# Kernel tuning notes

Measured on AMD Instinct MI355X. Metric: run time of the kernel, lower is better.

Reference implementation:

```python
import jax, jax.numpy as jnp
import numpy as np

INPUT_DIM = 362
HIDDEN = 256
STYLE_NUM = 60
OUTFIT_NUM = 49710
BATCH = 16384


def setup_inputs() -> dict:
    key = jax.random.key(0)
    ks = jax.random.split(key, 12)
    f32 = jnp.float32
    return {
        "i_feature": jax.random.normal(ks[0], (BATCH, INPUT_DIM), f32),
        "j_feature": jax.random.normal(ks[1], (BATCH, INPUT_DIM), f32),
        "k_feature": jax.random.normal(ks[2], (BATCH, INPUT_DIM), f32),
        # top_emb / bottom_emb Linear params (stored transposed: x @ W + b)
        "W_top": jax.random.normal(ks[3], (INPUT_DIM, HIDDEN), f32) * 0.05,
        "b_top": jnp.zeros((HIDDEN,), f32),
        "W_bot": jax.random.normal(ks[4], (INPUT_DIM, HIDDEN), f32) * 0.05,
        "b_bot": jnp.zeros((HIDDEN,), f32),
        # NMF factors (forward relu_'s them in place; we relu on use)
        "P_nmf": jax.random.normal(ks[5], (2 * INPUT_DIM, STYLE_NUM), f32),
        "N_nmf": jax.random.normal(ks[6], (2 * INPUT_DIM, STYLE_NUM), f32),
        "H1_nmf": jax.random.normal(ks[7], (STYLE_NUM, OUTFIT_NUM), f32),
        "H2_nmf": jax.random.normal(ks[8], (STYLE_NUM, OUTFIT_NUM), f32),
        "matirx_pos": jax.random.uniform(ks[9], (2 * INPUT_DIM, OUTFIT_NUM), f32),
        "matirx_neg": jax.random.uniform(ks[10], (2 * INPUT_DIM, OUTFIT_NUM), f32),
    }


def _emb(x, W, b):
    # nn.Sequential(Linear, Sigmoid)
    return jax.nn.sigmoid(x @ W + b)


def _style_score(i_f, j_f, styles, W_top, b_top, W_bot, b_bot):
    # Vectorized version of the per-sample loop:
    # squared-distance argmin codebook lookup + gather + rowwise dot.
    outfit = jnp.concatenate([i_f, j_f], axis=1)  # [B, 2D]
    # mean over feature dim of (x - s)^2; constant 1/(2D) scale does not change argmin
    d2 = (jnp.sum(outfit * outfit, axis=1, keepdims=True)
          - 2.0 * (outfit @ styles)
          + jnp.sum(styles * styles, axis=0, keepdims=True))  # [B, S]
    idx = jnp.argmin(d2, axis=1)                               # [B]
    sel = styles.T[idx]                                        # [B, 2D] gather
    top, bot = sel[:, :INPUT_DIM], sel[:, INPUT_DIM:]
    # diag(matmul) == rowwise dot
    return jnp.sum(_emb(top, W_top, b_top) * _emb(bot, W_bot, b_bot), axis=1)  # [B]


def reference(i_feature, j_feature, k_feature, W_top, b_top, W_bot, b_bot,
              P_nmf, N_nmf, H1_nmf, H2_nmf, matirx_pos, matirx_neg):
    Ti = _emb(i_feature, W_top, b_top)   # [B, H]
    Bj = _emb(j_feature, W_bot, b_bot)   # [B, H]
    Bk = _emb(k_feature, W_bot, b_bot)   # [B, H]
    # torch.diag(matmul(Ti, Bj.T)) == rowwise dot (avoids [B,B] intermediate)
    ij_score = jnp.sum(Ti * Bj, axis=1)  # [B]
    ik_score = jnp.sum(Ti * Bk, axis=1)  # [B]

    # forward does relu_ on .data before use
    P = jnp.maximum(P_nmf, 0.0)
    N = jnp.maximum(N_nmf, 0.0)
    H1 = jnp.maximum(H1_nmf, 0.0)
    H2 = jnp.maximum(H2_nmf, 0.0)

    style_ij = _style_score(i_feature, j_feature, P, W_top, b_top, W_bot, b_bot)
    style_ik = _style_score(i_feature, k_feature, N, W_top, b_top, W_bot, b_bot)

    # -mean(log(sigmoid(d))) computed stably
    loss1 = -jnp.mean(jax.nn.log_sigmoid(ij_score - ik_score))
    loss2 = -jnp.mean(jax.nn.log_sigmoid(style_ij - style_ik))
    loss3 = jnp.mean(jnp.square(matirx_pos - P @ H1)
                     + jnp.square(matirx_neg - N @ H2))
    loss = loss1 + loss2 + 0.1 * loss3

    ij_ik = jnp.stack([ij_score, ik_score], axis=1)  # [B, 2]
    auc = jnp.mean((jnp.argmax(ij_ik, axis=1) == 0).astype(jnp.float32))
    return (loss, loss1, loss2, loss3, auc)
```

## Files before the change

kernel.cpp:

```cpp
#include <hip/hip_runtime.h>
#include <math.h>

#define BATCH 16384
#define IND   362
#define KP    384
#define HID   256
#define STY   60
#define NOUT  49710
#define OUTP  49920
#define D2    724
#define D2P   768

#define NB_SS   120
#define NB_HR   3120
#define NB_CW   768
#define NB_CPN  384
#define NB_CF   9216
#define NB_PREP (NB_SS + NB_HR + NB_CW + NB_CPN + NB_CF)

#define NB_HH   16
#define NB_PPB  2
#define NB_HEAD (NB_HH + NB_PPB)
#define N_DT    46
#define N_OC    24
#define OCHUNK  2080
#define NB_M    (2 * N_DT * N_OC)
#define NB_EMB  1024
#define NB_SA   512
#define NB_MAIN (NB_HEAD + NB_M + NB_EMB + NB_SA)

typedef __bf16 bf16x8 __attribute__((ext_vector_type(8)));
typedef float  floatx4 __attribute__((ext_vector_type(4)));
typedef float  floatx2 __attribute__((ext_vector_type(2)));

__device__ inline floatx4 mfma16(bf16x8 a, bf16x8 b, floatx4 c) {
  return __builtin_amdgcn_mfma_f32_16x16x32_bf16(a, b, c, 0, 0, 0);
}

__device__ inline unsigned short f32_to_bf16(float x) {
  unsigned int u = __float_as_uint(x);
  unsigned int r = (u + 0x7FFFu + ((u >> 16) & 1u)) >> 16;
  return (unsigned short)r;
}

__device__ inline float sigm_fast(float x) { return 1.0f / (1.0f + __expf(-x)); }
__device__ inline float softplusf(float z) { return fmaxf(z, 0.0f) + log1pf(expf(-fabsf(z))); }

__global__ __launch_bounds__(256) void k_prep(
    const float* __restrict__ fi, const float* __restrict__ fj, const float* __restrict__ fk,
    const float* __restrict__ Wt, const float* __restrict__ btop,
    const float* __restrict__ Wb, const float* __restrict__ bbot,
    const float* __restrict__ Pn, const float* __restrict__ Nn,
    const float* __restrict__ H1, const float* __restrict__ H2,
    unsigned short* __restrict__ fbf, unsigned short* __restrict__ wbfT,
    unsigned short* __restrict__ pnbfT, unsigned short* __restrict__ hrows,
    float* __restrict__ ss, float* __restrict__ cn) {
  __shared__ float sel[D2];
  __shared__ float shr[4];
  int b = blockIdx.x;
  int t = threadIdx.x;

  if (b < NB_SS) {
    int s  = b % STY;
    int mt = b / STY;
    const float* M = mt ? Nn : Pn;
    float cnp = 0.0f;
    for (int d = t; d < D2; d += 256) {
      float v = fmaxf(M[(size_t)d * STY + s], 0.0f);
      sel[d] = v;
      cnp += v * v;
    }
    __syncthreads();
    float at = btop[t], ab = bbot[t];
    for (int d = 0; d < IND; d++) at = fmaf(sel[d],       Wt[(size_t)d * HID + t], at);
    for (int d = 0; d < IND; d++) ab = fmaf(sel[IND + d], Wb[(size_t)d * HID + t], ab);
    float prod = (1.0f / (1.0f + expf(-at))) * (1.0f / (1.0f + expf(-ab)));
    for (int off = 32; off > 0; off >>= 1) prod += __shfl_xor(prod, off);
    if ((t & 63) == 0) shr[t >> 6] = prod;
    __syncthreads();
    if (t == 0) ss[mt * 64 + s] = shr[0] + shr[1] + shr[2] + shr[3];
    __syncthreads();
    for (int off = 32; off > 0; off >>= 1) cnp += __shfl_xor(cnp, off);
    if ((t & 63) == 0) shr[t >> 6] = cnp;
    __syncthreads();
    if (t == 0) cn[mt * 64 + s] = shr[0] + shr[1] + shr[2] + shr[3];
    return;
  }
  b -= NB_SS;

  if (b < NB_HR) {
    int e = (b * 256 + t) * 8;
    int row = e / OUTP;
    int o = e - row * OUTP;
    int s = row & 63;
    int mm = row >> 6;
    const float* H = mm ? H2 : H1;
    unsigned short* dst = hrows + (size_t)row * OUTP + o;
    unsigned int wv[4];
    if (s < STY && o + 8 <= NOUT) {
      const float* src = H + (size_t)s * NOUT + o;
      #pragma unroll
      for (int ee = 0; ee < 4; ee++) {
        floatx2 v = *(const floatx2*)(src + 2 * ee);
        wv[ee] = (unsigned)f32_to_bf16(fmaxf(v[0], 0.0f)) |
                 ((unsigned)f32_to_bf16(fmaxf(v[1], 0.0f)) << 16);
      }
    } else {
      #pragma unroll
      for (int ee = 0; ee < 4; ee++) {
        float lo = (s < STY && o + 2 * ee     < NOUT) ? fmaxf(H[(size_t)s * NOUT + o + 2 * ee],     0.0f) : 0.0f;
        float hi = (s < STY && o + 2 * ee + 1 < NOUT) ? fmaxf(H[(size_t)s * NOUT + o + 2 * ee + 1], 0.0f) : 0.0f;
        wv[ee] = (unsigned)f32_to_bf16(lo) | ((unsigned)f32_to_bf16(hi) << 16);
      }
    }
    uint4 v; v.x = wv[0]; v.y = wv[1]; v.z = wv[2]; v.w = wv[3];
    *(uint4*)dst = v;
    return;
  }
  b -= NB_HR;

  if (b < NB_CW) {
    int idx = b * 256 + t;
    int k = idx % KP;
    int rem = idx / KP;
    int h = rem % HID;
    int mm = rem / HID;
    const float* W = mm ? Wb : Wt;
    wbfT[idx] = f32_to_bf16(k < IND ? W[(size_t)k * HID + h] : 0.0f);
    return;
  }
  b -= NB_CW;

  if (b < NB_CPN) {
    int u = b * 256 + t;
    int s = u & 63;
    int v = u >> 6;
    int m = (v >= D2P) ? 1 : 0;
    int d = v - m * D2P;
    const float* M = m ? Nn : Pn;
    float x = (d < D2 && s < STY) ? fmaxf(M[(size_t)d * STY + s], 0.0f) : 0.0f;
    unsigned short bb = f32_to_bf16(x);
    int k = (d < IND) ? d : (d < D2 ? d + 22 : (d < 746 ? d - IND : d));
    pnbfT[((size_t)m * 64 + s) * D2P + k] = bb;
    return;
  }
  b -= NB_CPN;

  {
    long u = (long)b * 256 + t;
    int g = (int)(u % 48);
    long rf = u / 48;
    int row = (int)(rf % BATCH);
    int f = (int)(rf / BATCH);
    const float* src = (f == 0) ? fi : (f == 1 ? fj : fk);
    int d0 = g * 8;
    const float* sp = src + (size_t)row * IND + d0;
    unsigned int wv[4];
    #pragma unroll
    for (int e = 0; e < 4; e++) {
      int dd = d0 + 2 * e;
      float lo = (dd < IND)     ? sp[2 * e]     : 0.0f;
      float hi = (dd + 1 < IND) ? sp[2 * e + 1] : 0.0f;
      wv[e] = (unsigned)f32_to_bf16(lo) | ((unsigned)f32_to_bf16(hi) << 16);
    }
    uint4 v; v.x = wv[0]; v.y = wv[1]; v.z = wv[2]; v.w = wv[3];
    *(uint4*)(fbf + ((size_t)f * BATCH + row) * KP + d0) = v;
  }
}

__global__ __launch_bounds__(256, 4) void k_main(
    const unsigned short* __restrict__ fbf, const unsigned short* __restrict__ wbfT,
    const unsigned short* __restrict__ pnbfT, const unsigned short* __restrict__ hrows,
    const float* __restrict__ btop, const float* __restrict__ bbot,
    const float* __restrict__ cn, const float* __restrict__ ss,
    const float* __restrict__ mp, const float* __restrict__ mneg,
    const float* __restrict__ Pn, const float* __restrict__ Nn,
    float* __restrict__ sIJ, float* __restrict__ sIK,
    float* __restrict__ stIJ, float* __restrict__ stIK,
    float* __restrict__ HHb, float* __restrict__ PPb,
    float* __restrict__ partial) {
  __shared__ float shp[4];
  __shared__ float red[4096];
  int w = threadIdx.x >> 6, lane = threadIdx.x & 63;
  int m = lane & 15, q = lane >> 4;
  int b = blockIdx.x;

  if (b < NB_HEAD) {
    bool isPP = (b >= NB_HH);
    int mat, chunk, nsteps, stride;
    const unsigned short* Rb;
    if (!isPP) { mat = b >> 3; chunk = b & 7; Rb = hrows + (size_t)mat * 64 * OUTP; stride = OUTP; nsteps = 195; }
    else       { mat = b - NB_HH; chunk = 0; Rb = pnbfT + (size_t)mat * 64 * D2P;  stride = D2P;  nsteps = 24;  }
    const unsigned short* Rm = Rb + (size_t)m * stride;

    floatx4 acc[4][4];
    #pragma unroll
    for (int a2 = 0; a2 < 4; a2++)
      #pragma unroll
      for (int b2 = 0; b2 < 4; b2++) acc[a2][b2] = (floatx4){0.f, 0.f, 0.f, 0.f};

    bf16x8 hc[4], hn[4];
    auto LD = [&](int j, bf16x8* h) {
      int k = (chunk * nsteps + j) * 32 + q * 8;
      #pragma unroll
      for (int st = 0; st < 4; st++)
        h[st] = *(const bf16x8*)(Rm + (size_t)(st * 16) * stride + k);
    };
    int j = w;
    LD(j, hc);
    for (; j < nsteps; j += 4) {
      if (j + 4 < nsteps) LD(j + 4, hn);
      #pragma unroll
      for (int a2 = 0; a2 < 4; a2++)
        #pragma unroll
        for (int b2 = 0; b2 < 4; b2++)
          acc[a2][b2] = mfma16(hc[a2], hc[b2], acc[a2][b2]);
      #pragma unroll
      for (int st = 0; st < 4; st++) hc[st] = hn[st];
    }
    for (int idx = threadIdx.x; idx < 4096; idx += 256) red[idx] = 0.f;
    __syncthreads();
    #pragma unroll
    for (int a2 = 0; a2 < 4; a2++)
      #pragma unroll
      for (int b2 = 0; b2 < 4; b2++)
        #pragma unroll
        for (int r = 0; r < 4; r++)
          atomicAdd(&red[(a2 * 16 + q * 4 + r) * 64 + b2 * 16 + m], acc[a2][b2][r]);
    __syncthreads();
    float* dst = (isPP ? PPb : HHb) + (size_t)mat * 4096;
    for (int idx = threadIdx.x; idx < 4096; idx += 256) atomicAdd(&dst[idx], red[idx]);
    return;
  }
  b -= NB_HEAD;

  if (b < NB_M) {
    int dt  = b % N_DT;
    int r   = b / N_DT;
    int oc  = r % N_OC;
    int mat = r / N_OC;
    int d0 = dt * 16, o0 = oc * OCHUNK;
    bool full = (o0 + OCHUNK <= NOUT);
    int d = d0 + m;
    bool rowok = (d < D2);
    const float* Mrow = (mat ? mneg : mp) + (size_t)d * NOUT;
    const unsigned short* Hbase = hrows + ((size_t)mat * 64 + m) * OUTP;

    floatx4 acc[4];
    #pragma unroll
    for (int st = 0; st < 4; st++) acc[st] = (floatx4){0.f, 0.f, 0.f, 0.f};
    float msq = 0.0f;

    floatx2 mc[4], mnx[4];
    bf16x8  hc[4], hn[4];

    auto LOADM = [&](int j, floatx2* dst) {
      int o = o0 + j * 32 + q * 8;
      if (rowok) {
        const float* Mr = Mrow + o;
        if (full) {
          dst[0] = *(const floatx2*)(Mr);
          dst[1] = *(const floatx2*)(Mr + 2);
          dst[2] = *(const floatx2*)(Mr + 4);
          dst[3] = *(const floatx2*)(Mr + 6);
        } else {
          #pragma unroll
          for (int e = 0; e < 4; e++) {
            floatx2 v = {0.f, 0.f};
            if (o + 2 * e     < NOUT) v[0] = Mr[2 * e];
            if (o + 2 * e + 1 < NOUT) v[1] = Mr[2 * e + 1];
            dst[e] = v;
          }
        }
      } else {
        #pragma unroll
        for (int e = 0; e < 4; e++) dst[e] = (floatx2){0.f, 0.f};
      }
    };
    auto LOADH = [&](int j, bf16x8* h) {
      int o = o0 + j * 32 + q * 8;
      #pragma unroll
      for (int st = 0; st < 4; st++)
        h[st] = *(const bf16x8*)(Hbase + (size_t)(st * 16) * OUTP + o);
    };

    LOADM(w, mc);
    LOADH(w, hc);
    for (int j = w; j < 65; j += 4) {
      if (j + 4 < 65) { LOADM(j + 4, mnx); LOADH(j + 4, hn); }
      union { unsigned int u32[4]; bf16x8 v; } cv;
      #pragma unroll
      for (int e = 0; e < 4; e++) {
        msq = fmaf(mc[e][0], mc[e][0], msq);
        msq = fmaf(mc[e][1], mc[e][1], msq);
        cv.u32[e] = (unsigned)f32_to_bf16(mc[e][0]) | ((unsigned)f32_to_bf16(mc[e][1]) << 16);
      }
      bf16x8 af = cv.v;
      #pragma unroll
      for (int st = 0; st < 4; st++) acc[st] = mfma16(af, hc[st], acc[st]);
      #pragma unroll
      for (int e = 0; e < 4; e++) mc[e] = mnx[e];
      #pragma unroll
      for (int st = 0; st < 4; st++) hc[st] = hn[st];
    }

    const float* PM = mat ? Nn : Pn;
    float t2 = 0.0f;
    #pragma unroll
    for (int st = 0; st < 4; st++) {
      int s = st * 16 + m;
      if (s < STY) {
        #pragma unroll
        for (int rg = 0; rg < 4; rg++) {
          int dd = d0 + q * 4 + rg;
          if (dd < D2) {
            float pv = fmaxf(PM[(size_t)dd * STY + s], 0.0f);
            t2 = fmaf(pv, acc[st][rg], t2);
          }
        }
      }
    }
    float local = msq - 2.0f * t2;
    for (int off = 32; off > 0; off >>= 1) local += __shfl_xor(local, off);
    if (lane == 0) shp[w] = local;
    __syncthreads();
    if (threadIdx.x == 0) partial[b] = shp[0] + shp[1] + shp[2] + shp[3];
    return;
  }
  b -= NB_M;

  if (b < NB_EMB) {
    int r0 = (b & 255) * 64 + w * 16;
    int hb = (b >> 8) * 64;
    const unsigned short* fi = fbf + (size_t)(r0 + m) * KP + q * 8;
    const unsigned short* fj = fi + (size_t)BATCH * KP;
    const unsigned short* fk = fj + (size_t)BATCH * KP;
    floatx4 accI[4], accJ[4], accK[4];
    #pragma unroll
    for (int nt = 0; nt < 4; nt++) {
      accI[nt] = (floatx4){0.f, 0.f, 0.f, 0.f};
      accJ[nt] = (floatx4){0.f, 0.f, 0.f, 0.f};
      accK[nt] = (floatx4){0.f, 0.f, 0.f, 0.f};
    }
    for (int kc = 0; kc < 12; kc++) {
      bf16x8 ai = *(const bf16x8*)(fi + kc * 32);
      bf16x8 aj = *(const bf16x8*)(fj + kc * 32);
      bf16x8 ak = *(const bf16x8*)(fk + kc * 32);
      #pragma unroll
      for (int nt = 0; nt < 4; nt++) {
        int n = hb + nt * 16 + m;
        const unsigned short* wp = wbfT + (size_t)n * KP + kc * 32 + q * 8;
        bf16x8 bt8 = *(const bf16x8*)(wp);
        bf16x8 bb8 = *(const bf16x8*)(wp + (size_t)HID * KP);
        accI[nt] = mfma16(ai, bt8, accI[nt]);
        accJ[nt] = mfma16(aj, bb8, accJ[nt]);
        accK[nt] = mfma16(ak, bb8, accK[nt]);
      }
    }
    float sij[4] = {0.f, 0.f, 0.f, 0.f}, sik[4] = {0.f, 0.f, 0.f, 0.f};
    #pragma unroll
    for (int nt = 0; nt < 4; nt++) {
      int n = hb + nt * 16 + m;
      float vbt = btop[n], vbb = bbot[n];
      #pragma unroll
      for (int reg = 0; reg < 4; reg++) {
        float ti = sigm_fast(accI[nt][reg] + vbt);
        float tj = sigm_fast(accJ[nt][reg] + vbb);
        float tk = sigm_fast(accK[nt][reg] + vbb);
        sij[reg] += ti * tj;
        sik[reg] += ti * tk;
      }
    }
    #pragma unroll
    for (int reg = 0; reg < 4; reg++) {
      for (int off = 1; off < 16; off <<= 1) {
        sij[reg] += __shfl_xor(sij[reg], off);
        sik[reg] += __shfl_xor(sik[reg], off);
      }
    }
    if (m == 0) {
      #pragma unroll
      for (int reg = 0; reg < 4; reg++) {
        int row = r0 + q * 4 + reg;
        atomicAdd(&sIJ[row], sij[reg]);
        atomicAdd(&sIK[row], sik[reg]);
      }
    }
    return;
  }
  b -= NB_EMB;

  {
    int mat = w & 1;
    int r0 = b * 32 + (w >> 1) * 16;
    const unsigned short* fA = fbf + (size_t)(r0 + m) * KP + q * 8;
    const unsigned short* fB = fA + (size_t)(1 + mat) * BATCH * KP;
    const unsigned short* Bp = pnbfT + (size_t)mat * 64 * D2P + q * 8;
    floatx4 acc[4];
    #pragma unroll
    for (int nt = 0; nt < 4; nt++) acc[nt] = (floatx4){0.f, 0.f, 0.f, 0.f};
    for (int kc = 0; kc < 24; kc++) {
      bf16x8 a = (kc < 12) ? *(const bf16x8*)(fA + kc * 32)
                           : *(const bf16x8*)(fB + (kc - 12) * 32);
      #pragma unroll
      for (int nt = 0; nt < 4; nt++) {
        bf16x8 bb = *(const bf16x8*)(Bp + (size_t)(nt * 16 + m) * D2P + kc * 32);
        acc[nt] = mfma16(a, bb, acc[nt]);
      }
    }
    const float* cnm = cn + mat * 64;
    float bv[4]; int bi[4];
    #pragma unroll
    for (int reg = 0; reg < 4; reg++) { bv[reg] = __builtin_inff(); bi[reg] = 1 << 30; }
    #pragma unroll
    for (int nt = 0; nt < 4; nt++) {
      int s = nt * 16 + m;
      float c = cnm[s & 63];
      #pragma unroll
      for (int reg = 0; reg < 4; reg++) {
        float d2 = (s < STY) ? (c - 2.0f * acc[nt][reg]) : __builtin_inff();
        if (d2 < bv[reg] || (d2 == bv[reg] && s < bi[reg])) { bv[reg] = d2; bi[reg] = s; }
      }
    }
    for (int off = 1; off < 16; off <<= 1) {
      #pragma unroll
      for (int reg = 0; reg < 4; reg++) {
        float ov = __shfl_xor(bv[reg], off);
        int   oi = __shfl_xor(bi[reg], off);
        if (ov < bv[reg] || (ov == bv[reg] && oi < bi[reg])) { bv[reg] = ov; bi[reg] = oi; }
      }
    }
    if (m == 0) {
      float* dst = mat ? stIK : stIJ;
      const float* ssm = ss + mat * 64;
      #pragma unroll
      for (int reg = 0; reg < 4; reg++) dst[r0 + q * 4 + reg] = ssm[bi[reg]];
    }
  }
}

__global__ __launch_bounds__(256) void k_final(
    const float* __restrict__ sIJ, const float* __restrict__ sIK,
    const float* __restrict__ stIJ, const float* __restrict__ stIK,
    const float* __restrict__ l3partial,
    const float* __restrict__ HHb, const float* __restrict__ PPb,
    float* __restrict__ out) {
  int t = threadIdx.x;
  float l1 = 0.f, l2 = 0.f, ac = 0.f;
  for (int r = t; r < BATCH; r += 256) {
    float dij = sIJ[r] - sIK[r];
    l1 += softplusf(-dij);
    if (dij >= 0.0f) ac += 1.0f;
    float dst = stIJ[r] - stIK[r];
    l2 += softplusf(-dst);
  }
  double l3 = 0.0;
  for (int p = t; p < NB_M; p += 256) l3 += (double)l3partial[p];
  for (int idx = t; idx < 8192; idx += 256) l3 += (double)HHb[idx] * (double)PPb[idx];
  __shared__ float sh1[4], sh2[4], sh3[4];
  __shared__ double sh4[4];
  for (int off = 32; off > 0; off >>= 1) {
    l1 += __shfl_xor(l1, off);
    l2 += __shfl_xor(l2, off);
    ac += __shfl_xor(ac, off);
    l3 += __shfl_xor(l3, off);
  }
  if ((t & 63) == 0) { sh1[t >> 6] = l1; sh2[t >> 6] = l2; sh3[t >> 6] = ac; sh4[t >> 6] = l3; }
  __syncthreads();
  if (t == 0) {
    double L1 = 0, L2 = 0, AC = 0, L3 = 0;
    for (int i = 0; i < 4; i++) { L1 += sh1[i]; L2 += sh2[i]; AC += sh3[i]; L3 += sh4[i]; }
    L1 /= BATCH; L2 /= BATCH; AC /= BATCH;
    L3 /= ((double)D2 * (double)NOUT);
    out[0] = (float)(L1 + L2 + 0.1 * L3);
    out[1] = (float)L1;
    out[2] = (float)L2;
    out[3] = (float)L3;
    out[4] = (float)AC;
  }
}

extern "C" void kernel_launch(void* const* d_in, const int* in_sizes, int n_in,
                              void* d_out, int out_size, void* d_ws, size_t ws_size,
                              hipStream_t stream) {
  (void)in_sizes; (void)n_in; (void)out_size; (void)ws_size;
  const float* i_f  = (const float*)d_in[0];
  const float* j_f  = (const float*)d_in[1];
  const float* k_f  = (const float*)d_in[2];
  const float* W_t  = (const float*)d_in[3];
  const float* b_t  = (const float*)d_in[4];
  const float* W_b  = (const float*)d_in[5];
  const float* b_b  = (const float*)d_in[6];
  const float* P_n  = (const float*)d_in[7];
  const float* N_n  = (const float*)d_in[8];
  const float* H1   = (const float*)d_in[9];
  const float* H2   = (const float*)d_in[10];
  const float* Mp   = (const float*)d_in[11];
  const float* Mn   = (const float*)d_in[12];
  float* out = (float*)d_out;
  char* ws = (char*)d_ws;

  const size_t OFF_FBF   = 0;
  const size_t OFF_WBFT  = OFF_FBF   + (size_t)3 * BATCH * KP * 2;
  const size_t OFF_PNBFT = OFF_WBFT  + (size_t)2 * HID * KP * 2;
  const size_t OFF_HROWS = OFF_PNBFT + (size_t)2 * 64 * D2P * 2;
  const size_t OFF_SIJ   = OFF_HROWS + (size_t)2 * 64 * OUTP * 2;
  const size_t OFF_SIK   = OFF_SIJ   + (size_t)BATCH * 4;
  const size_t OFF_HH    = OFF_SIK   + (size_t)BATCH * 4;
  const size_t OFF_PP    = OFF_HH    + (size_t)2 * 4096 * 4;
  const size_t OFF_STIJ  = OFF_PP    + (size_t)2 * 4096 * 4;
  const size_t OFF_STIK  = OFF_STIJ  + (size_t)BATCH * 4;
  const size_t OFF_SS    = OFF_STIK  + (size_t)BATCH * 4;
  const size_t OFF_CN    = OFF_SS    + 512;
  const size_t OFF_L3P   = OFF_CN    + 512;

  unsigned short* fbf   = (unsigned short*)(ws + OFF_FBF);
  unsigned short* wbfT  = (unsigned short*)(ws + OFF_WBFT);
  unsigned short* pnbfT = (unsigned short*)(ws + OFF_PNBFT);
  unsigned short* hrows = (unsigned short*)(ws + OFF_HROWS);
  float*  sIJ  = (float*)(ws + OFF_SIJ);
  float*  sIK  = (float*)(ws + OFF_SIK);
  float*  HHb  = (float*)(ws + OFF_HH);
  float*  PPb  = (float*)(ws + OFF_PP);
  float*  stIJ = (float*)(ws + OFF_STIJ);
  float*  stIK = (float*)(ws + OFF_STIK);
  float*  ss   = (float*)(ws + OFF_SS);
  float*  cn   = (float*)(ws + OFF_CN);
  float*  l3p  = (float*)(ws + OFF_L3P);

  hipMemsetAsync(ws + OFF_SIJ, 0, (size_t)BATCH * 4 * 2 + (size_t)4 * 4096 * 4, stream);

  k_prep<<<NB_PREP, 256, 0, stream>>>(i_f, j_f, k_f, W_t, b_t, W_b, b_b,
                                      P_n, N_n, H1, H2,
                                      fbf, wbfT, pnbfT, hrows, ss, cn);
  k_main<<<NB_MAIN, 256, 0, stream>>>(fbf, wbfT, pnbfT, hrows,
                                      b_t, b_b, cn, ss, Mp, Mn, P_n, N_n,
                                      sIJ, sIK, stIJ, stIK, HHb, PPb, l3p);
  k_final<<<1, 256, 0, stream>>>(sIJ, sIK, stIJ, stIK, l3p, HHb, PPb, out);
}
```

Baseline: 662.8 us.

## Restructure NMF loss blocks into 64-column strips with register-resident H tiles

The M·H cross-term blocks now each own a 64-column strip of the outfit dimension and loop over all 724 feature rows. The H tile stays in registers for the whole strip, and M rows are double-buffered in pairs. Previously each block tiled 16 rows by 2080 columns and reloaded H for every row tile. OUTP padding grows to 51200, and the HH/PP Gram head blocks move to the end of the grid so the streaming blocks launch first. Dropping the occupancy hint from launch_bounds gives more registers per thread, at the risk of fewer waves being resident to hide memory latency.

Result: slower. 909.9 us (+37.3%).

```diff
diff --git a/kernel.cpp b/kernel.cpp
--- a/kernel.cpp
+++ b/kernel.cpp
@@ -7,27 +7,26 @@
 #define HID   256
 #define STY   60
 #define NOUT  49710
-#define OUTP  49920
+#define OUTP  51200
 #define D2    724
 #define D2P   768
 
 #define NB_SS   120
-#define NB_HR   3120
+#define NB_HR   3200
 #define NB_CW   768
 #define NB_CPN  384
 #define NB_CF   9216
 #define NB_PREP (NB_SS + NB_HR + NB_CW + NB_CPN + NB_CF)
 
+#define NSTRIP  777
+#define NB_MB   (2 * NSTRIP)
+#define NPAIR   23
+#define NB_EMB  1024
+#define NB_SA   512
 #define NB_HH   16
 #define NB_PPB  2
 #define NB_HEAD (NB_HH + NB_PPB)
-#define N_DT    46
-#define N_OC    24
-#define OCHUNK  2080
-#define NB_M    (2 * N_DT * N_OC)
-#define NB_EMB  1024
-#define NB_SA   512
-#define NB_MAIN (NB_HEAD + NB_M + NB_EMB + NB_SA)
+#define NB_MAIN (NB_MB + NB_EMB + NB_SA + NB_HEAD)
 
 typedef __bf16 bf16x8 __attribute__((ext_vector_type(8)));
 typedef float  floatx4 __attribute__((ext_vector_type(4)));
@@ -168,7 +167,7 @@
   }
 }
 
-__global__ __launch_bounds__(256, 4) void k_main(
+__global__ __launch_bounds__(256) void k_main(
     const unsigned short* __restrict__ fbf, const unsigned short* __restrict__ wbfT,
     const unsigned short* __restrict__ pnbfT, const unsigned short* __restrict__ hrows,
     const float* __restrict__ btop, const float* __restrict__ bbot,
@@ -179,155 +178,112 @@
     float* __restrict__ stIJ, float* __restrict__ stIK,
     float* __restrict__ HHb, float* __restrict__ PPb,
     float* __restrict__ partial) {
-  __shared__ float shp[4];
   __shared__ float red[4096];
   int w = threadIdx.x >> 6, lane = threadIdx.x & 63;
   int m = lane & 15, q = lane >> 4;
   int b = blockIdx.x;
 
-  if (b < NB_HEAD) {
-    bool isPP = (b >= NB_HH);
-    int mat, chunk, nsteps, stride;
-    const unsigned short* Rb;
-    if (!isPP) { mat = b >> 3; chunk = b & 7; Rb = hrows + (size_t)mat * 64 * OUTP; stride = OUTP; nsteps = 195; }
-    else       { mat = b - NB_HH; chunk = 0; Rb = pnbfT + (size_t)mat * 64 * D2P;  stride = D2P;  nsteps = 24;  }
-    const unsigned short* Rm = Rb + (size_t)m * stride;
-
-    floatx4 acc[4][4];
-    #pragma unroll
-    for (int a2 = 0; a2 < 4; a2++)
-      #pragma unroll
-      for (int b2 = 0; b2 < 4; b2++) acc[a2][b2] = (floatx4){0.f, 0.f, 0.f, 0.f};
-
-    bf16x8 hc[4], hn[4];
-    auto LD = [&](int j, bf16x8* h) {
-      int k = (chunk * nsteps + j) * 32 + q * 8;
-      #pragma unroll
-      for (int st = 0; st < 4; st++)
-        h[st] = *(const bf16x8*)(Rm + (size_t)(st * 16) * stride + k);
-    };
-    int j = w;
-    LD(j, hc);
-    for (; j < nsteps; j += 4) {
-      if (j + 4 < nsteps) LD(j + 4, hn);
-      #pragma unroll
-      for (int a2 = 0; a2 < 4; a2++)
+  if (b < NB_MB) {
+    int mat   = b & 1;
+    int strip = b >> 1;
+    int o0 = strip * 64;
+    bool full = (o0 + 64 <= NOUT);
+    const float* Mbase = mat ? mneg : mp;
+    const float* PM    = mat ? Nn : Pn;
+
+    bf16x8 h[4][2];
+    #pragma unroll
+    for (int st = 0; st < 4; st++)
+      #pragma unroll
+      for (int kc = 0; kc < 2; kc++)
+        h[st][kc] = *(const bf16x8*)(hrows + ((size_t)mat * 64 + st * 16 + m) * OUTP
+                                     + o0 + kc * 32 + q * 8);
+
+    float msq = 0.0f, t2 = 0.0f;
+    floatx2 B0[16], B1[16];
+
+    auto LOADP = [&](int pt, floatx2* B) {
+      #pragma unroll
+      for (int tt = 0; tt < 2; tt++) {
+        int d = pt * 32 + tt * 16 + m;
+        bool ok = (pt < NPAIR) && (d < D2);
+        const float* Mrow = Mbase + (size_t)d * NOUT + o0;
         #pragma unroll
-        for (int b2 = 0; b2 < 4; b2++)
-          acc[a2][b2] = mfma16(hc[a2], hc[b2], acc[a2][b2]);
-      #pragma unroll
-      for (int st = 0; st < 4; st++) hc[st] = hn[st];
-    }
-    for (int idx = threadIdx.x; idx < 4096; idx += 256) red[idx] = 0.f;
-    __syncthreads();
-    #pragma unroll
-    for (int a2 = 0; a2 < 4; a2++)
-      #pragma unroll
-      for (int b2 = 0; b2 < 4; b2++)
-        #pragma unroll
-        for (int r = 0; r < 4; r++)
-          atomicAdd(&red[(a2 * 16 + q * 4 + r) * 64 + b2 * 16 + m], acc[a2][b2][r]);
-    __syncthreads();
-    float* dst = (isPP ? PPb : HHb) + (size_t)mat * 4096;
-    for (int idx = threadIdx.x; idx < 4096; idx += 256) atomicAdd(&dst[idx], red[idx]);
-    return;
-  }
-  b -= NB_HEAD;
-
-  if (b < NB_M) {
-    int dt  = b % N_DT;
-    int r   = b / N_DT;
-    int oc  = r % N_OC;
-    int mat = r / N_OC;
-    int d0 = dt * 16, o0 = oc * OCHUNK;
-    bool full = (o0 + OCHUNK <= NOUT);
-    int d = d0 + m;
-    bool rowok = (d < D2);
-    const float* Mrow = (mat ? mneg : mp) + (size_t)d * NOUT;
-    const unsigned short* Hbase = hrows + ((size_t)mat * 64 + m) * OUTP;
-
-    floatx4 acc[4];
-    #pragma unroll
-    for (int st = 0; st < 4; st++) acc[st] = (floatx4){0.f, 0.f, 0.f, 0.f};
-    float msq = 0.0f;
-
-    floatx2 mc[4], mnx[4];
-    bf16x8  hc[4], hn[4];
-
-    auto LOADM = [&](int j, floatx2* dst) {
-      int o = o0 + j * 32 + q * 8;
-      if (rowok) {
-        const float* Mr = Mrow + o;
-        if (full) {
-          dst[0] = *(const floatx2*)(Mr);
-          dst[1] = *(const floatx2*)(Mr + 2);
-          dst[2] = *(const floatx2*)(Mr + 4);
-          dst[3] = *(const floatx2*)(Mr + 6);
-        } else {
+        for (int kc = 0; kc < 2; kc++) {
           #pragma unroll
           for (int e = 0; e < 4; e++) {
+            int oo = kc * 32 + q * 8 + 2 * e;
             floatx2 v = {0.f, 0.f};
-            if (o + 2 * e     < NOUT) v[0] = Mr[2 * e];
-            if (o + 2 * e + 1 < NOUT) v[1] = Mr[2 * e + 1];
-            dst[e] = v;
+            if (ok) {
+              if (full) {
+                v = *(const floatx2*)(Mrow + oo);
+              } else {
+                if (o0 + oo     < NOUT) v[0] = Mrow[oo];
+                if (o0 + oo + 1 < NOUT) v[1] = Mrow[oo + 1];
+              }
+            }
+            B[(tt * 2 + kc) * 4 + e] = v;
           }
         }
-      } else {
+      }
+    };
+
+    auto COMP = [&](const floatx2* B, int pt) {
+      #pragma unroll
+      for (int tt = 0; tt < 2; tt++) {
+        floatx4 acc[4];
         #pragma unroll
-        for (int e = 0; e < 4; e++) dst[e] = (floatx2){0.f, 0.f};
-      }
-    };
-    auto LOADH = [&](int j, bf16x8* h) {
-      int o = o0 + j * 32 + q * 8;
-      #pragma unroll
-      for (int st = 0; st < 4; st++)
-        h[st] = *(const bf16x8*)(Hbase + (size_t)(st * 16) * OUTP + o);
-    };
-
-    LOADM(w, mc);
-    LOADH(w, hc);
-    for (int j = w; j < 65; j += 4) {
-      if (j + 4 < 65) { LOADM(j + 4, mnx); LOADH(j + 4, hn); }
-      union { unsigned int u32[4]; bf16x8 v; } cv;
-      #pragma unroll
-      for (int e = 0; e < 4; e++) {
-        msq = fmaf(mc[e][0], mc[e][0], msq);
-        msq = fmaf(mc[e][1], mc[e][1], msq);
-        cv.u32[e] = (unsigned)f32_to_bf16(mc[e][0]) | ((unsigned)f32_to_bf16(mc[e][1]) << 16);
-      }
-      bf16x8 af = cv.v;
-      #pragma unroll
-      for (int st = 0; st < 4; st++) acc[st] = mfma16(af, hc[st], acc[st]);
-      #pragma unroll
-      for (int e = 0; e < 4; e++) mc[e] = mnx[e];
-      #pragma unroll
-      for (int st = 0; st < 4; st++) hc[st] = hn[st];
-    }
-
-    const float* PM = mat ? Nn : Pn;
-    float t2 = 0.0f;
-    #pragma unroll
-    for (int st = 0; st < 4; st++) {
-      int s = st * 16 + m;
-      if (s < STY) {
+        for (int st = 0; st < 4; st++) acc[st] = (floatx4){0.f, 0.f, 0.f, 0.f};
         #pragma unroll
-        for (int rg = 0; rg < 4; rg++) {
-          int dd = d0 + q * 4 + rg;
-          if (dd < D2) {
-            float pv = fmaxf(PM[(size_t)dd * STY + s], 0.0f);
-            t2 = fmaf(pv, acc[st][rg], t2);
+        for (int kc = 0; kc < 2; kc++) {
+          union { unsigned int u[4]; bf16x8 v; } cv;
+          #pragma unroll
+          for (int e = 0; e < 4; e++) {
+            floatx2 tv = B[(tt * 2 + kc) * 4 + e];
+            msq = fmaf(tv[0], tv[0], msq);
+            msq = fmaf(tv[1], tv[1], msq);
+            cv.u[e] = (unsigned)f32_to_bf16(tv[0]) | ((unsigned)f32_to_bf16(tv[1]) << 16);
+          }
+          #pragma unroll
+          for (int st = 0; st < 4; st++) acc[st] = mfma16(cv.v, h[st][kc], acc[st]);
+        }
+        #pragma unroll
+        for (int st = 0; st < 4; st++) {
+          int s = st * 16 + m;
+          if (s < STY) {
+            #pragma unroll
+            for (int rg = 0; rg < 4; rg++) {
+              int dd = pt * 32 + tt * 16 + q * 4 + rg;
+              if (dd < D2) {
+                float pv = fmaxf(PM[(size_t)dd * STY + s], 0.0f);
+                t2 = fmaf(pv, acc[st][rg], t2);
+              }
+            }
           }
         }
       }
-    }
+    };
+
+    int pt0 = w;
+    LOADP(pt0, B0);
+    LOADP(pt0 + 4, B1);
+    for (int pt = pt0; pt < NPAIR; pt += 8) {
+      COMP(B0, pt);
+      if (pt + 8 < NPAIR) LOADP(pt + 8, B0);
+      if (pt + 4 < NPAIR) {
+        COMP(B1, pt + 4);
+        if (pt + 12 < NPAIR) LOADP(pt + 12, B1);
+      }
+    }
+
     float local = msq - 2.0f * t2;
     for (int off = 32; off > 0; off >>= 1) local += __shfl_xor(local, off);
-    if (lane == 0) shp[w] = local;
-    __syncthreads();
-    if (threadIdx.x == 0) partial[b] = shp[0] + shp[1] + shp[2] + shp[3];
-    return;
-  }
-  b -= NB_M;
+    if (lane == 0) red[w] = local;
+    __syncthreads();
+    if (threadIdx.x == 0) partial[blockIdx.x] = red[0] + red[1] + red[2] + red[3];
+    return;
+  }
+  b -= NB_MB;
 
   if (b < NB_EMB) {
     int r0 = (b & 255) * 64 + w * 16;
@@ -390,7 +346,7 @@
   }
   b -= NB_EMB;
 
-  {
+  if (b < NB_SA) {
     int mat = w & 1;
     int r0 = b * 32 + (w >> 1) * 16;
     const unsigned short* fA = fbf + (size_t)(r0 + m) * KP + q * 8;
@@ -436,6 +392,55 @@
       #pragma unroll
       for (int reg = 0; reg < 4; reg++) dst[r0 + q * 4 + reg] = ssm[bi[reg]];
     }
+    return;
+  }
+  b -= NB_SA;
+
+  {
+    bool isPP = (b >= NB_HH);
+    int mat, chunk, nsteps, stride;
+    const unsigned short* Rb;
+    if (!isPP) { mat = b >> 3; chunk = b & 7; Rb = hrows + (size_t)mat * 64 * OUTP; stride = OUTP; nsteps = 200; }
+    else       { mat = b - NB_HH; chunk = 0; Rb = pnbfT + (size_t)mat * 64 * D2P;  stride = D2P;  nsteps = 24;  }
+    const unsigned short* Rm = Rb + (size_t)m * stride;
+
+    floatx4 acc[4][4];
+    #pragma unroll
+    for (int a2 = 0; a2 < 4; a2++)
+      #pragma unroll
+      for (int b2 = 0; b2 < 4; b2++) acc[a2][b2] = (floatx4){0.f, 0.f, 0.f, 0.f};
+
+    bf16x8 hc[4], hn[4];
+    auto LD = [&](int j, bf16x8* hh) {
+      int k = (chunk * nsteps + j) * 32 + q * 8;
+      #pragma unroll
+      for (int st = 0; st < 4; st++)
+        hh[st] = *(const bf16x8*)(Rm + (size_t)(st * 16) * stride + k);
+    };
+    int j = w;
+    LD(j, hc);
+    for (; j < nsteps; j += 4) {
+      if (j + 4 < nsteps) LD(j + 4, hn);
+      #pragma unroll
+      for (int a2 = 0; a2 < 4; a2++)
+        #pragma unroll
+        for (int b2 = 0; b2 < 4; b2++)
+          acc[a2][b2] = mfma16(hc[a2], hc[b2], acc[a2][b2]);
+      #pragma unroll
+      for (int st = 0; st < 4; st++) hc[st] = hn[st];
+    }
+    for (int idx = threadIdx.x; idx < 4096; idx += 256) red[idx] = 0.f;
+    __syncthreads();
+    #pragma unroll
+    for (int a2 = 0; a2 < 4; a2++)
+      #pragma unroll
+      for (int b2 = 0; b2 < 4; b2++)
+        #pragma unroll
+        for (int r = 0; r < 4; r++)
+          atomicAdd(&red[(a2 * 16 + q * 4 + r) * 64 + b2 * 16 + m], acc[a2][b2][r]);
+    __syncthreads();
+    float* dst = (isPP ? PPb : HHb) + (size_t)mat * 4096;
+    for (int idx = threadIdx.x; idx < 4096; idx += 256) atomicAdd(&dst[idx], red[idx]);
   }
 }
 
@@ -455,7 +460,7 @@
     l2 += softplusf(-dst);
   }
   double l3 = 0.0;
-  for (int p = t; p < NB_M; p += 256) l3 += (double)l3partial[p];
+  for (int p = t; p < NB_MB; p += 256) l3 += (double)l3partial[p];
   for (int idx = t; idx < 8192; idx += 256) l3 += (double)HHb[idx] * (double)PPb[idx];
   __shared__ float sh1[4], sh2[4], sh3[4];
   __shared__ double sh4[4];
```
